# Kernel tuning notes

Measured on AMD Instinct MI355X. Metric: run time of the kernel, lower is better.

## Reference

```python
import jax, jax.numpy as jnp
import numpy as np

NUM_HEADS, NUM_KV, HEAD_DIM, WIDTH = 4, 1, 256, 1024
MASK_FILL = -2.3819763e38


def _apply_rope(x, positions, max_wavelength=10000.0):
    # x: [B, T, N, H], positions: [B, T]
    d = x.shape[-1]
    freq_exp = (2.0 / d) * jnp.arange(d // 2, dtype=jnp.float32)
    timescale = max_wavelength ** freq_exp                      # [H/2]
    radians = positions[..., None].astype(jnp.float32) / timescale  # [B, T, H/2]
    radians = radians[..., None, :]                             # [B, T, 1, H/2]
    sin, cos = jnp.sin(radians), jnp.cos(radians)
    x1, x2 = jnp.split(x, 2, axis=-1)
    out = jnp.concatenate([x1 * cos - x2 * sin, x2 * cos + x1 * sin], axis=-1)
    return out.astype(x.dtype)


def _rmsnorm(x, scale):
    var = jnp.mean(jnp.square(x.astype(jnp.float32)), axis=-1, keepdims=True)
    normed = x * jax.lax.rsqrt(var + 1e-6)
    return (normed * (1 + scale)).astype(x.dtype)


def setup_inputs() -> dict:
    key = jax.random.key(0)
    ks = jax.random.split(key, 7)
    B, T, S = 8, 512, 2048
    return {
        "x": jax.random.normal(ks[0], (B, T, WIDTH), jnp.float32),
        "mem_seq": jax.random.normal(ks[1], (B, S, WIDTH), jnp.float32),
        "mem_mask": jax.random.randint(ks[2], (B, S), 0, 2).astype(bool),
        "rms_scale": jax.random.normal(ks[3], (WIDTH,), jnp.float32) * 0.02,
        "q_w": jax.random.normal(ks[4], (NUM_HEADS, WIDTH, HEAD_DIM), jnp.float32) / np.sqrt(WIDTH),
        "kv_w": jax.random.normal(ks[5], (2, NUM_KV, WIDTH, HEAD_DIM), jnp.float32) / np.sqrt(WIDTH),
        "out_w": jax.random.normal(ks[6], (NUM_HEADS, HEAD_DIM, WIDTH), jnp.float32) / np.sqrt(NUM_HEADS * HEAD_DIM),
    }


def reference(x, mem_seq, mem_mask, rms_scale, q_w, kv_w, out_w):
    B, S, _ = mem_seq.shape
    T = x.shape[1]
    G = NUM_HEADS // NUM_KV  # query heads per kv head

    xn = _rmsnorm(x, rms_scale)          # shared RMSNorm params
    mn = _rmsnorm(mem_seq, rms_scale)

    q = jnp.einsum("BTD,NDH->BTNH", xn, q_w)          # [B,T,4,256]
    kv = jnp.einsum("BSD,cKDH->cBSKH", mn, kv_w)      # [2,B,S,1,256]
    k, v = kv[0], kv[1]

    q_pos = jnp.broadcast_to(jnp.arange(S, T + S), (B, T))
    k_pos = jnp.broadcast_to(jnp.arange(S), (B, S))
    q = _apply_rope(q, q_pos) * (HEAD_DIM ** -0.5)
    k = _apply_rope(k, k_pos)

    q = q.reshape(B, T, NUM_KV, G, HEAD_DIM)
    logits = jnp.einsum("BTKGH,BSKH->BKGTS", q, k, preferred_element_type=jnp.float32)
    masked = jnp.where(mem_mask[:, None, None, None, :], logits, MASK_FILL)
    probs = jax.nn.softmax(masked, axis=-1).astype(x.dtype)
    enc = jnp.einsum("BKGTS,BSKH->BTKGH", probs, v).reshape(B, T, NUM_HEADS, HEAD_DIM)
    return jnp.einsum("BTNH,NHD->BTD", enc, out_w)
```

## Files before the change

### kernel.cpp

```cpp
#include <hip/hip_runtime.h>
#include <stdint.h>

typedef __bf16   bf16x8 __attribute__((ext_vector_type(8)));
typedef float    f32x4  __attribute__((ext_vector_type(4)));
typedef float    f32x16 __attribute__((ext_vector_type(16)));
typedef uint16_t u16x8  __attribute__((ext_vector_type(8)));
typedef uint16_t u16x4  __attribute__((ext_vector_type(4)));
typedef uint32_t u32x4  __attribute__((ext_vector_type(4)));

#define DEVFN static __device__ __forceinline__

DEVFN uint16_t f2bf(float f){
  uint32_t u = __builtin_bit_cast(uint32_t, f);
  u += 0x7fffu + ((u >> 16) & 1u);
  return (uint16_t)(u >> 16);
}
DEVFN float bf2f(uint16_t h){
  return __builtin_bit_cast(float, (uint32_t)h << 16);
}
DEVFN bf16x8 ldbf8(const uint16_t* p){
  return __builtin_bit_cast(bf16x8, *(const u16x8*)p);
}
DEVFN void gl16(const void* g, void* l){
  __builtin_amdgcn_global_load_lds((__attribute__((address_space(1))) void*)g,
                                   (__attribute__((address_space(3))) void*)l,
                                   16, 0, 0);
}
DEVFN f32x4 mfma16(bf16x8 a, bf16x8 b, f32x4 c){
  return __builtin_amdgcn_mfma_f32_16x16x32_bf16(a, b, c, 0, 0, 0);
}
DEVFN f32x16 mfma32(bf16x8 a, bf16x8 b, f32x16 c){
  return __builtin_amdgcn_mfma_f32_32x32x16_bf16(a, b, c, 0, 0, 0);
}
DEVFN uint32_t cvtpk(float lo, float hi){
  uint32_t r;
  asm("v_cvt_pk_bf16_f32 %0, %1, %2" : "=v"(r) : "v"(lo), "v"(hi));
  return r;
}
DEVFN void plswap(uint32_t &x, uint32_t &y){
  asm("v_permlane32_swap_b32 %0, %1" : "+v"(x), "+v"(y));
}
DEVFN int permcol(int j){
  return (((j & 127) >> 4) << 5) + (((j >> 7) & 1) << 4) + (j & 15);
}
DEVFN void fastsc(float rad, float& sn, float& cs){
  float rev = rad * 0.15915494309189535f;
  rev = __builtin_amdgcn_fractf(rev);
  sn = __builtin_amdgcn_sinf(rev);
  cs = __builtin_amdgcn_cosf(rev);
}

__global__ void detect_mask_k(const uint32_t* m, int* flag){
  int i = blockIdx.x * 256 + threadIdx.x;
  uint32_t v = m[i];
  int notint   = (v > 1u) ? 1 : 0;
  int notfloat = (v != 0u && v != 0x3F800000u) ? 2 : 0;
  int bits = notint | notfloat;
  if (__any(bits)){
    int agg = bits;
    agg |= __shfl_xor(agg, 1);  agg |= __shfl_xor(agg, 2);
    agg |= __shfl_xor(agg, 4);  agg |= __shfl_xor(agg, 8);
    agg |= __shfl_xor(agg, 16); agg |= __shfl_xor(agg, 32);
    if ((threadIdx.x & 63) == 0) atomicOr(flag, agg);
  }
}

__global__ __launch_bounds__(256) void fused_pre_k(const float* __restrict__ x,
                                                   const float* __restrict__ mem,
                                                   uint16_t* __restrict__ xn,
                                                   uint16_t* __restrict__ mn,
                                                   const float* __restrict__ scale,
                                                   const float* __restrict__ qw,
                                                   const float* __restrict__ kvw,
                                                   const float* __restrict__ ow,
                                                   uint16_t* __restrict__ wq,
                                                   uint16_t* __restrict__ wkv,
                                                   uint16_t* __restrict__ wout){
  int bid = blockIdx.x;
  if (bid < 20480){
    int row = bid;
    const float* in; uint16_t* out; int r0;
    if (row < 4096){ in = x;  out = xn; r0 = row; }
    else           { in = mem; out = mn; r0 = row - 4096; }
    const float4* ip = (const float4*)(in + (size_t)r0 * 1024);
    float4 v = ip[threadIdx.x];
    float ss = v.x*v.x + v.y*v.y + v.z*v.z + v.w*v.w;
    #pragma unroll
    for (int off = 1; off < 64; off <<= 1) ss += __shfl_xor(ss, off);
    __shared__ float wsum[4];
    if ((threadIdx.x & 63) == 0) wsum[threadIdx.x >> 6] = ss;
    __syncthreads();
    float r = rsqrtf((wsum[0] + wsum[1] + wsum[2] + wsum[3]) * (1.0f/1024.0f) + 1e-6f);
    float4 sc = ((const float4*)scale)[threadIdx.x];
    u16x4 o;
    o[0] = f2bf(v.x * r * (1.0f + sc.x));
    o[1] = f2bf(v.y * r * (1.0f + sc.y));
    o[2] = f2bf(v.z * r * (1.0f + sc.z));
    o[3] = f2bf(v.w * r * (1.0f + sc.w));
    *(u16x4*)(out + (size_t)r0 * 1024 + threadIdx.x * 4) = o;
  } else {
    int t = bid - 20480;
    int z = t >> 10, rem = t & 1023;
    int r0 = (rem >> 5) * 32, c0 = (rem & 31) * 32;
    const float* in; uint16_t* out; int rs, C;
    bool perm;
    if (z < 4)      { in = qw  + z*262144;     out = wq  + z*262144;     rs = 256;  C = 256;  perm = true;  }
    else if (z < 6) { in = kvw + (z-4)*262144; out = wkv + (z-4)*262144; rs = 256;  C = 256;  perm = (z == 4); }
    else            { in = ow;                 out = wout;               rs = 1024; C = 1024; perm = false; }
    if (c0 >= C) return;
    __shared__ float tt[32][33];
    int tx = threadIdx.x & 31, ty = threadIdx.x >> 5;
    #pragma unroll
    for (int i = 0; i < 4; ++i)
      tt[ty + 8*i][tx] = in[(size_t)(r0 + ty + 8*i) * rs + c0 + tx];
    __syncthreads();
    #pragma unroll
    for (int i = 0; i < 4; ++i){
      int c = c0 + ty + 8*i;
      int pc = perm ? permcol(c) : c;
      out[(size_t)pc * 1024 + r0 + tx] = f2bf(tt[tx][ty + 8*i]);
    }
  }
}

#define GEMM_BODY(A_, Bt_, K_)                                                  \
  __shared__ __align__(16) uint16_t As[128*64];                                 \
  __shared__ __align__(16) uint16_t Bs[128*64];                                 \
  f32x4 acc[4][4] = {};                                                         \
  {                                                                             \
    const int K = (K_);                                                         \
    _Pragma("unroll 1")                                                         \
    for (int k0 = 0; k0 < K; k0 += 64){                                         \
      __syncthreads();                                                          \
      _Pragma("unroll")                                                         \
      for (int it = 0; it < 4; ++it){                                           \
        int ob = it * 4096 + tid * 16;                                          \
        int row = ob >> 7;                                                      \
        int col = (ob & 127) ^ ((row & 7) << 4);                                \
        gl16((const char*)(A_)  + ((size_t)(m0 + row) * K + k0) * 2 + col,      \
             (char*)As + it * 4096 + wid * 1024);                               \
        gl16((const char*)(Bt_) + ((size_t)(n0 + row) * K + k0) * 2 + col,      \
             (char*)Bs + it * 4096 + wid * 1024);                               \
      }                                                                         \
      __syncthreads();                                                          \
      bf16x8 af[2][4], bfr[2][4];                                               \
      _Pragma("unroll")                                                         \
      for (int ks = 0; ks < 2; ++ks){                                           \
        _Pragma("unroll")                                                       \
        for (int m = 0; m < 4; ++m)                                             \
          af[ks][m]  = ldbf8(&As[(wr*64 + m*16 + lr) * 64 +                     \
                                 ((ks*32 + lq*8) ^ ((lr & 7) << 3))]);          \
        _Pragma("unroll")                                                       \
        for (int n = 0; n < 4; ++n)                                             \
          bfr[ks][n] = ldbf8(&Bs[(wc*64 + n*16 + lr) * 64 +                     \
                                 ((ks*32 + lq*8) ^ ((lr & 7) << 3))]);          \
      }                                                                         \
      _Pragma("unroll")                                                         \
      for (int ks = 0; ks < 2; ++ks)                                            \
        _Pragma("unroll")                                                       \
        for (int m = 0; m < 4; ++m)                                             \
          _Pragma("unroll")                                                     \
          for (int n = 0; n < 4; ++n)                                           \
            acc[m][n] = mfma16(af[ks][m], bfr[ks][n], acc[m][n]);               \
    }                                                                           \
  }

__global__ __launch_bounds__(256) void gemm_qkv_k(const uint16_t* __restrict__ xn,
                                                  const uint16_t* __restrict__ mn,
                                                  const uint16_t* __restrict__ wq,
                                                  const uint16_t* __restrict__ wkv,
                                                  uint16_t* __restrict__ qb,
                                                  uint16_t* __restrict__ kb,
                                                  uint16_t* __restrict__ vt3){
  int bx = blockIdx.x;
  bool isq = bx < 256;
  const uint16_t *A, *Bt;
  int n0, m0;
  if (isq){
    int m = (bx & 7) + 8 * (bx >> 6);
    int n = (bx >> 3) & 7;
    A = xn; Bt = wq;  n0 = n * 128;  m0 = m * 128;
  } else {
    int b2 = bx - 256;
    int m = (b2 & 7) + 8 * (b2 >> 5);
    int n = (b2 >> 3) & 3;
    A = mn; Bt = wkv; n0 = n * 128; m0 = m * 128;
  }
  int tid = threadIdx.x, lane = tid & 63, wid = tid >> 6;
  int wr = wid >> 1, wc = wid & 1;
  int lr = lane & 15, lq = lane >> 4;
  GEMM_BODY(A, Bt, 1024)
  if (isq){
    #pragma unroll
    for (int m = 0; m < 4; ++m){
      int gr0 = m0 + wr*64 + m*16 + lq*4;
      #pragma unroll
      for (int np = 0; np < 2; ++np){
        int gcl = n0 + wc*64 + (2*np)*16 + lr;
        int j = (((gcl & 255) >> 5) << 4) + (gcl & 15);
        float inv = exp2f((float)j * (-13.287712379549449f / 128.0f));
        #pragma unroll
        for (int r = 0; r < 4; ++r){
          float rad = (float)(2048 + ((gr0 + r) & 511)) * inv;
          float sn, cs; fastsc(rad, sn, cs);
          float x1 = acc[m][2*np][r], x2 = acc[m][2*np + 1][r];
          qb[(size_t)(gr0 + r) * 1024 + gcl]      = f2bf((x1*cs - x2*sn) * 0.0625f);
          qb[(size_t)(gr0 + r) * 1024 + gcl + 16] = f2bf((x2*cs + x1*sn) * 0.0625f);
        }
      }
    }
  } else if (n0 < 256){
    #pragma unroll
    for (int m = 0; m < 4; ++m){
      int gr0 = m0 + wr*64 + m*16 + lq*4;
      #pragma unroll
      for (int np = 0; np < 2; ++np){
        int gcl = n0 + wc*64 + (2*np)*16 + lr;
        int j = ((gcl >> 5) << 4) + (gcl & 15);
        float inv = exp2f((float)j * (-13.287712379549449f / 128.0f));
        #pragma unroll
        for (int r = 0; r < 4; ++r){
          float rad = (float)((gr0 + r) & 2047) * inv;
          float sn, cs; fastsc(rad, sn, cs);
          float x1 = acc[m][2*np][r], x2 = acc[m][2*np + 1][r];
          kb[(size_t)(gr0 + r) * 256 + gcl]      = f2bf(x1*cs - x2*sn);
          kb[(size_t)(gr0 + r) * 256 + gcl + 16] = f2bf(x2*cs + x1*sn);
        }
      }
    }
  } else {
    #pragma unroll
    for (int m = 0; m < 4; ++m)
      #pragma unroll
      for (int n = 0; n < 4; ++n){
        int gr0 = m0 + wr*64 + m*16 + lq*4;
        int gc  = n0 + wc*64 + n*16 + lr;
        int h = gc - 256, bb = gr0 >> 11, s0 = gr0 & 2047;
        int st = s0 >> 5, sc = (s0 >> 3) & 3, s8 = s0 & 7;
        u16x4 pk;
        #pragma unroll
        for (int r = 0; r < 4; ++r) pk[r] = f2bf(acc[m][n][r]);
        *(u16x4*)&vt3[((((size_t)bb*64 + st)*4 + sc)*256 + h)*8 + s8] = pk;
      }
  }
}

__global__ __launch_bounds__(256) void gemm_out_k(const uint16_t* __restrict__ A,
                                                  const uint16_t* __restrict__ Bt,
                                                  float* __restrict__ Cf){
  int bx = blockIdx.x;
  int m = (bx & 7) + 8 * (bx >> 6);
  int n = (bx >> 3) & 7;
  int n0 = n * 128, m0 = m * 128;
  int tid = threadIdx.x, lane = tid & 63, wid = tid >> 6;
  int wr = wid >> 1, wc = wid & 1;
  int lr = lane & 15, lq = lane >> 4;
  GEMM_BODY(A, Bt, 1024)
  #pragma unroll
  for (int mm = 0; mm < 4; ++mm)
    #pragma unroll
    for (int nn = 0; nn < 4; ++nn){
      int gr0 = m0 + wr*64 + mm*16 + lq*4;
      int gc  = n0 + wc*64 + nn*16 + lr;
      #pragma unroll
      for (int r = 0; r < 4; ++r) Cf[(size_t)(gr0 + r) * 1024 + gc] = acc[mm][nn][r];
    }
}

__global__ __launch_bounds__(512, 2) void attn_k(const uint16_t* __restrict__ Q,
                                                 const uint16_t* __restrict__ Kb,
                                                 const uint16_t* __restrict__ Vt3,
                                                 const void* __restrict__ mask,
                                                 const int* __restrict__ flag,
                                                 uint16_t* __restrict__ po,
                                                 uint16_t* __restrict__ po3,
                                                 float* __restrict__ pm,
                                                 float* __restrict__ pl){
  int bx = blockIdx.x;
  int b = bx & 7, qt = (bx >> 3) & 7, sh = bx >> 6;
  int tid = threadIdx.x, lane = tid & 63, wid = tid >> 6;
  int n = wid & 3, qs = wid >> 2;
  int lc = lane & 31, hi = lane >> 5;
  __shared__ __align__(16) uint16_t Ks[3*32*256];
  __shared__ __align__(16) uint16_t Vs[3*4*256*8];
  __shared__ uint32_t mask_lds[16];

  int sbeg = sh * 512;
  {
    int f = *flag;
    int gi = b*2048 + sbeg + tid;
    bool on;
    if ((f & 1) == 0)      on = ((const int*)mask)[gi]    != 0;
    else if ((f & 2) == 0) on = ((const float*)mask)[gi]  != 0.0f;
    else                   on = ((const uint8_t*)mask)[gi] != 0;
    unsigned long long bal = __ballot(on);
    if (lane == 0){
      mask_lds[wid*2]     = (uint32_t)bal;
      mask_lds[wid*2 + 1] = (uint32_t)(bal >> 32);
    }
  }

  int t0w = qt*64 + qs*32;
  bf16x8 qf[16];
  {
    const uint16_t* qp = Q + (size_t)(b*512 + t0w + lc) * 1024 + n*256 + hi*8;
    #pragma unroll
    for (int kc = 0; kc < 16; ++kc) qf[kc] = ldbf8(qp + kc*16);
  }
  f32x16 o[8] = {};
  float mrow = -1e30f, lrow = 0.0f;

  auto STAGE = [&](int buf, int s0){
    const char* vsrc = (const char*)Vt3 + ((size_t)(b*64 + (s0 >> 5))) * 16384;
    #pragma unroll
    for (int it = 0; it < 2; ++it){
      int ob = it*8192 + tid*16;
      int krow = ob >> 9;
      int kcol = (ob & 511) ^ ((krow & 7) << 4);
      gl16((const char*)Kb + ((size_t)(b*2048 + s0 + krow) * 256) * 2 + kcol,
           (char*)Ks + buf*16384 + it*8192 + wid*1024);
      gl16(vsrc + ob,
           (char*)Vs + buf*16384 + it*8192 + wid*1024);
    }
  };

  STAGE(0, sbeg);
  STAGE(1, sbeg + 32);

  #pragma unroll 1
  for (int t = 0; t < 16; ++t){
    if (t == 0)      asm volatile("s_waitcnt vmcnt(4) lgkmcnt(0)" ::: "memory");
    else if (t < 15) asm volatile("s_waitcnt vmcnt(4)" ::: "memory");
    else             asm volatile("s_waitcnt vmcnt(0)" ::: "memory");
    __builtin_amdgcn_s_barrier();
    asm volatile("" ::: "memory");
    if (t < 14) STAGE((t+2)%3, sbeg + (t+2)*32);

    const uint16_t* ksb = Ks + (t%3)*8192;
    const uint16_t* vsb = Vs + (t%3)*8192;

    f32x16 sacc = {};
    __builtin_amdgcn_s_setprio(1);
    #pragma unroll
    for (int kc = 0; kc < 16; ++kc){
      bf16x8 ak = ldbf8(&ksb[lc*256 + ((kc*16 + hi*8) ^ ((lc & 7) << 3))]);
      sacc = mfma32(ak, qf[kc], sacc);
    }
    __builtin_amdgcn_s_setprio(0);

    uint32_t mw = mask_lds[t];
    int sb4 = hi * 4;
    float p[16];
    float mx = -1e30f;
    #pragma unroll
    for (int r = 0; r < 16; ++r){
      int sr = (r & 3) + 8*(r >> 2) + sb4;
      float v = ((mw >> sr) & 1u) ? sacc[r] : -1e30f;
      p[r] = v;
      mx = fmaxf(mx, v);
    }
    mx = fmaxf(mx, __shfl_xor(mx, 32));
    if (__any(mx > mrow + 8.0f)){
      float mn = fmaxf(mrow, mx);
      float scl = __expf(mrow - mn);
      mrow = mn; lrow *= scl;
      #pragma unroll
      for (int ht = 0; ht < 8; ++ht) o[ht] *= scl;
    }
    float rs = 0.0f;
    #pragma unroll
    for (int r = 0; r < 16; ++r){ p[r] = __expf(p[r] - mrow); rs += p[r]; }
    rs += __shfl_xor(rs, 32);
    lrow += rs;

    uint32_t w0, w1, w2, w3, w4, w5, w6, w7;
    w0 = cvtpk(p[0], p[1]);   w2 = cvtpk(p[4], p[5]);   plswap(w0, w2);
    w1 = cvtpk(p[2], p[3]);   w3 = cvtpk(p[6], p[7]);   plswap(w1, w3);
    w4 = cvtpk(p[8], p[9]);   w6 = cvtpk(p[12], p[13]); plswap(w4, w6);
    w5 = cvtpk(p[10], p[11]); w7 = cvtpk(p[14], p[15]); plswap(w5, w7);
    u32x4 t0v = {w0, w1, w2, w3};
    u32x4 t1v = {w4, w5, w6, w7};
    bf16x8 pa0 = __builtin_bit_cast(bf16x8, t0v);
    bf16x8 pa1 = __builtin_bit_cast(bf16x8, t1v);

    __builtin_amdgcn_s_setprio(1);
    #pragma unroll
    for (int ht = 0; ht < 8; ++ht){
      bf16x8 bv0 = ldbf8(&vsb[(size_t)hi*2048       + (ht*32 + lc)*8]);
      o[ht] = mfma32(pa0, bv0, o[ht]);
      bf16x8 bv1 = ldbf8(&vsb[(size_t)(2 + hi)*2048 + (ht*32 + lc)*8]);
      o[ht] = mfma32(pa1, bv1, o[ht]);
    }
    __builtin_amdgcn_s_setprio(0);
  }

  uint16_t* pop = (sh == 3) ? po3 : po + (size_t)sh * 4194304;
  #pragma unroll
  for (int ht = 0; ht < 8; ++ht)
    #pragma unroll
    for (int r = 0; r < 16; ++r){
      int qr = (r & 3) + 8*(r >> 2) + hi*4;
      pop[(size_t)(b*512 + t0w + qr)*1024 + n*256 + ht*32 + lc] = f2bf(o[ht][r]);
    }
  if (hi == 0){
    int mlidx = sh*16384 + (b*512 + t0w + lc)*4 + n;
    pm[mlidx] = mrow;
    pl[mlidx] = lrow;
  }
}

__global__ __launch_bounds__(256) void merge_k(const uint16_t* __restrict__ po,
                                               const uint16_t* __restrict__ po3,
                                               const float* __restrict__ pm,
                                               const float* __restrict__ pl,
                                               uint16_t* __restrict__ enc){
  int idx = blockIdx.x * 4 + (threadIdx.x >> 6);
  int lane = threadIdx.x & 63;
  int row = idx >> 2, n = idx & 3;
  float m = -1e30f;
  #pragma unroll
  for (int h = 0; h < 4; ++h) m = fmaxf(m, pm[h*16384 + idx]);
  float w[4], lsum = 0.0f;
  #pragma unroll
  for (int h = 0; h < 4; ++h){
    w[h] = __expf(pm[h*16384 + idx] - m);
    lsum += pl[h*16384 + idx] * w[h];
  }
  float inv = 1.0f / lsum;
  size_t off = (size_t)row*1024 + n*256 + lane*4;
  float acc[4] = {0.f, 0.f, 0.f, 0.f};
  #pragma unroll
  for (int h = 0; h < 4; ++h){
    const uint16_t* src = (h < 3) ? po + (size_t)h*4194304 + off : po3 + off;
    u16x4 a = *(const u16x4*)src;
    #pragma unroll
    for (int r = 0; r < 4; ++r) acc[r] += bf2f(a[r]) * w[h];
  }
  u16x4 ov;
  #pragma unroll
  for (int r = 0; r < 4; ++r) ov[r] = f2bf(acc[r] * inv);
  *(u16x4*)(enc + off) = ov;
}

extern "C" void kernel_launch(void* const* d_in, const int* in_sizes, int n_in,
                              void* d_out, int out_size, void* d_ws, size_t ws_size,
                              hipStream_t stream){
  const float* x    = (const float*)d_in[0];
  const float* mem  = (const float*)d_in[1];
  const void*  mask = d_in[2];
  const float* rms  = (const float*)d_in[3];
  const float* qw   = (const float*)d_in[4];
  const float* kvw  = (const float*)d_in[5];
  const float* ow   = (const float*)d_in[6];
  float* out = (float*)d_out;
  char* ws = (char*)d_ws;

  uint16_t* xn   = (uint16_t*)(ws + 0);
  uint16_t* enc  = (uint16_t*)(ws + 0);
  const size_t MB = 1ull << 20;
  uint16_t* qb   = (uint16_t*)(ws + 8*MB);
  uint16_t* kb   = (uint16_t*)(ws + 16*MB);
  uint16_t* vt3  = (uint16_t*)(ws + 24*MB);
  uint16_t* wq   = (uint16_t*)(ws + 32*MB);
  float*    pm   = (float*)   (ws + 32*MB);
  float*    pl   = (float*)   (ws + 32*MB + 262144);
  uint16_t* wkv  = (uint16_t*)(ws + 34*MB);
  uint16_t* wout = (uint16_t*)(ws + 35*MB);
  int*      flag = (int*)     (ws + 37*MB);
  uint16_t* mn   = (uint16_t*)(ws + 38*MB);
  uint16_t* po   = (uint16_t*)(ws + 38*MB);
  uint16_t* po3  = (uint16_t*)out;

  hipMemsetAsync(flag, 0, 4, stream);
  detect_mask_k<<<16, 256, 0, stream>>>((const uint32_t*)mask, flag);

  fused_pre_k<<<27648, 256, 0, stream>>>(x, mem, xn, mn, rms, qw, kvw, ow, wq, wkv, wout);

  gemm_qkv_k<<<768, 256, 0, stream>>>(xn, mn, wq, wkv, qb, kb, vt3);

  attn_k<<<256, 512, 0, stream>>>(qb, kb, vt3, mask, flag, po, po3, pm, pl);
  merge_k<<<4096, 256, 0, stream>>>(po, po3, pm, pl, enc);

  gemm_out_k<<<256, 256, 0, stream>>>(enc, wout, out);
}
```

Measured before the change: 161.1 us.

## Fuse split-KV merge into output GEMM and fold mask detection into prep

The separate merge kernel is removed. The output GEMM now computes the per-row combine weights from the partial max and sum values, then merges the four bf16 partial outputs while loading its A tile into LDS. The mask-format detection blocks are appended to the fused preprocessing launch, which drops one kernel launch. All four partials now live in workspace instead of borrowing the output buffer. In exchange, each A tile is merged again by every N-block (8x redundant partial reads), and the A loads become synchronous register loads instead of async global-to-LDS copies.

```diff
diff --git a/kernel.cpp b/kernel.cpp
--- a/kernel.cpp
+++ b/kernel.cpp
@@ -48,21 +48,6 @@
   rev = __builtin_amdgcn_fractf(rev);
   sn = __builtin_amdgcn_sinf(rev);
   cs = __builtin_amdgcn_cosf(rev);
-}
-
-__global__ void detect_mask_k(const uint32_t* m, int* flag){
-  int i = blockIdx.x * 256 + threadIdx.x;
-  uint32_t v = m[i];
-  int notint   = (v > 1u) ? 1 : 0;
-  int notfloat = (v != 0u && v != 0x3F800000u) ? 2 : 0;
-  int bits = notint | notfloat;
-  if (__any(bits)){
-    int agg = bits;
-    agg |= __shfl_xor(agg, 1);  agg |= __shfl_xor(agg, 2);
-    agg |= __shfl_xor(agg, 4);  agg |= __shfl_xor(agg, 8);
-    agg |= __shfl_xor(agg, 16); agg |= __shfl_xor(agg, 32);
-    if ((threadIdx.x & 63) == 0) atomicOr(flag, agg);
-  }
 }
 
 __global__ __launch_bounds__(256) void fused_pre_k(const float* __restrict__ x,
@@ -75,7 +60,9 @@
                                                    const float* __restrict__ ow,
                                                    uint16_t* __restrict__ wq,
                                                    uint16_t* __restrict__ wkv,
-                                                   uint16_t* __restrict__ wout){
+                                                   uint16_t* __restrict__ wout,
+                                                   const uint32_t* __restrict__ mask32,
+                                                   int* __restrict__ flag){
   int bid = blockIdx.x;
   if (bid < 20480){
     int row = bid;
@@ -98,7 +85,7 @@
     o[2] = f2bf(v.z * r * (1.0f + sc.z));
     o[3] = f2bf(v.w * r * (1.0f + sc.w));
     *(u16x4*)(out + (size_t)r0 * 1024 + threadIdx.x * 4) = o;
-  } else {
+  } else if (bid < 27648){
     int t = bid - 20480;
     int z = t >> 10, rem = t & 1023;
     int r0 = (rem >> 5) * 32, c0 = (rem & 31) * 32;
@@ -119,6 +106,19 @@
       int c = c0 + ty + 8*i;
       int pc = perm ? permcol(c) : c;
       out[(size_t)pc * 1024 + r0 + tx] = f2bf(tt[tx][ty + 8*i]);
+    }
+  } else {
+    int i = (bid - 27648) * 256 + threadIdx.x;
+    uint32_t v = mask32[i];
+    int notint   = (v > 1u) ? 1 : 0;
+    int notfloat = (v != 0u && v != 0x3F800000u) ? 2 : 0;
+    int bits = notint | notfloat;
+    if (__any(bits)){
+      int agg = bits;
+      agg |= __shfl_xor(agg, 1);  agg |= __shfl_xor(agg, 2);
+      agg |= __shfl_xor(agg, 4);  agg |= __shfl_xor(agg, 8);
+      agg |= __shfl_xor(agg, 16); agg |= __shfl_xor(agg, 32);
+      if ((threadIdx.x & 63) == 0) atomicOr(flag, agg);
     }
   }
 }
@@ -245,7 +245,9 @@
   }
 }
 
-__global__ __launch_bounds__(256) void gemm_out_k(const uint16_t* __restrict__ A,
+__global__ __launch_bounds__(256) void gemm_out_k(const uint16_t* __restrict__ po,
+                                                  const float* __restrict__ pm,
+                                                  const float* __restrict__ pl,
                                                   const uint16_t* __restrict__ Bt,
                                                   float* __restrict__ Cf){
   int bx = blockIdx.x;
@@ -255,7 +257,76 @@
   int tid = threadIdx.x, lane = tid & 63, wid = tid >> 6;
   int wr = wid >> 1, wc = wid & 1;
   int lr = lane & 15, lq = lane >> 4;
-  GEMM_BODY(A, Bt, 1024)
+  __shared__ __align__(16) uint16_t As[128*64];
+  __shared__ __align__(16) uint16_t Bs[128*64];
+  __shared__ float sc_lds[128][4][4];
+  f32x4 acc[4][4] = {};
+
+  for (int e = tid; e < 512; e += 256){
+    int row = e >> 2, hd = e & 3;
+    int gi = (m0 + row) * 4 + hd;
+    float pmv[4], plv[4], m4 = -1e30f;
+    #pragma unroll
+    for (int h = 0; h < 4; ++h){
+      pmv[h] = pm[h*16384 + gi];
+      plv[h] = pl[h*16384 + gi];
+      m4 = fmaxf(m4, pmv[h]);
+    }
+    float wv[4], ls = 0.0f;
+    #pragma unroll
+    for (int h = 0; h < 4; ++h){ wv[h] = __expf(pmv[h] - m4); ls += plv[h]*wv[h]; }
+    float inv = 1.0f / ls;
+    #pragma unroll
+    for (int h = 0; h < 4; ++h) sc_lds[row][hd][h] = wv[h] * inv;
+  }
+
+  #pragma unroll 1
+  for (int k0 = 0; k0 < 1024; k0 += 64){
+    __syncthreads();
+    int hd = k0 >> 8;
+    #pragma unroll
+    for (int it = 0; it < 4; ++it){
+      int ob = it * 4096 + tid * 16;
+      int row = ob >> 7;
+      int colb = ob & 127;
+      int scolb = colb ^ ((row & 7) << 4);
+      gl16((const char*)Bt + ((size_t)(n0 + row) * 1024 + k0) * 2 + scolb,
+           (char*)Bs + it * 4096 + wid * 1024);
+      size_t abase = ((size_t)(m0 + row) * 1024 + k0) * 2 + colb;
+      u16x8 pp0 = *(const u16x8*)((const char*)po                    + abase);
+      u16x8 pp1 = *(const u16x8*)((const char*)po + (size_t)8388608  + abase);
+      u16x8 pp2 = *(const u16x8*)((const char*)po + (size_t)16777216 + abase);
+      u16x8 pp3 = *(const u16x8*)((const char*)po + (size_t)25165824 + abase);
+      float s0_ = sc_lds[row][hd][0], s1_ = sc_lds[row][hd][1];
+      float s2_ = sc_lds[row][hd][2], s3_ = sc_lds[row][hd][3];
+      u16x8 mrg;
+      #pragma unroll
+      for (int e2 = 0; e2 < 8; ++e2){
+        float a = bf2f(pp0[e2])*s0_ + bf2f(pp1[e2])*s1_
+                + bf2f(pp2[e2])*s2_ + bf2f(pp3[e2])*s3_;
+        mrg[e2] = f2bf(a);
+      }
+      *(u16x8*)((char*)As + row * 128 + scolb) = mrg;
+    }
+    __syncthreads();
+    bf16x8 af[2][4], bfr[2][4];
+    #pragma unroll
+    for (int ks = 0; ks < 2; ++ks){
+      #pragma unroll
+      for (int mm = 0; mm < 4; ++mm)
+        af[ks][mm]  = ldbf8(&As[(wr*64 + mm*16 + lr) * 64 + ((ks*32 + lq*8) ^ ((lr & 7) << 3))]);
+      #pragma unroll
+      for (int nn = 0; nn < 4; ++nn)
+        bfr[ks][nn] = ldbf8(&Bs[(wc*64 + nn*16 + lr) * 64 + ((ks*32 + lq*8) ^ ((lr & 7) << 3))]);
+    }
+    #pragma unroll
+    for (int ks = 0; ks < 2; ++ks)
+      #pragma unroll
+      for (int mm = 0; mm < 4; ++mm)
+        #pragma unroll
+        for (int nn = 0; nn < 4; ++nn)
+          acc[mm][nn] = mfma16(af[ks][mm], bfr[ks][nn], acc[mm][nn]);
+  }
   #pragma unroll
   for (int mm = 0; mm < 4; ++mm)
     #pragma unroll
@@ -273,7 +344,6 @@
                                                  const void* __restrict__ mask,
                                                  const int* __restrict__ flag,
                                                  uint16_t* __restrict__ po,
-                                                 uint16_t* __restrict__ po3,
                                                  float* __restrict__ pm,
                                                  float* __restrict__ pl){
   int bx = blockIdx.x;
@@ -361,9 +431,9 @@
     }
     mx = fmaxf(mx, __shfl_xor(mx, 32));
     if (__any(mx > mrow + 8.0f)){
-      float mn = fmaxf(mrow, mx);
-      float scl = __expf(mrow - mn);
-      mrow = mn; lrow *= scl;
+      float mn2 = fmaxf(mrow, mx);
+      float scl = __expf(mrow - mn2);
+      mrow = mn2; lrow *= scl;
       #pragma unroll
       for (int ht = 0; ht < 8; ++ht) o[ht] *= scl;
     }
@@ -394,7 +464,7 @@
     __builtin_amdgcn_s_setprio(0);
   }
 
-  uint16_t* pop = (sh == 3) ? po3 : po + (size_t)sh * 4194304;
+  uint16_t* pop = po + (size_t)sh * 4194304;
   #pragma unroll
   for (int ht = 0; ht < 8; ++ht)
     #pragma unroll
@@ -407,39 +477,6 @@
     pm[mlidx] = mrow;
     pl[mlidx] = lrow;
   }
-}
-
-__global__ __launch_bounds__(256) void merge_k(const uint16_t* __restrict__ po,
-                                               const uint16_t* __restrict__ po3,
-                                               const float* __restrict__ pm,
-                                               const float* __restrict__ pl,
-                                               uint16_t* __restrict__ enc){
-  int idx = blockIdx.x * 4 + (threadIdx.x >> 6);
-  int lane = threadIdx.x & 63;
-  int row = idx >> 2, n = idx & 3;
-  float m = -1e30f;
-  #pragma unroll
-  for (int h = 0; h < 4; ++h) m = fmaxf(m, pm[h*16384 + idx]);
-  float w[4], lsum = 0.0f;
-  #pragma unroll
-  for (int h = 0; h < 4; ++h){
-    w[h] = __expf(pm[h*16384 + idx] - m);
-    lsum += pl[h*16384 + idx] * w[h];
-  }
-  float inv = 1.0f / lsum;
-  size_t off = (size_t)row*1024 + n*256 + lane*4;
-  float acc[4] = {0.f, 0.f, 0.f, 0.f};
-  #pragma unroll
-  for (int h = 0; h < 4; ++h){
-    const uint16_t* src = (h < 3) ? po + (size_t)h*4194304 + off : po3 + off;
-    u16x4 a = *(const u16x4*)src;
-    #pragma unroll
-    for (int r = 0; r < 4; ++r) acc[r] += bf2f(a[r]) * w[h];
-  }
-  u16x4 ov;
-  #pragma unroll
-  for (int r = 0; r < 4; ++r) ov[r] = f2bf(acc[r] * inv);
-  *(u16x4*)(enc + off) = ov;
 }
 
 extern "C" void kernel_launch(void* const* d_in, const int* in_sizes, int n_in,
@@ -456,7 +493,6 @@
   char* ws = (char*)d_ws;
 
   uint16_t* xn   = (uint16_t*)(ws + 0);
-  uint16_t* enc  = (uint16_t*)(ws + 0);
   const size_t MB = 1ull << 20;
   uint16_t* qb   = (uint16_t*)(ws + 8*MB);
   uint16_t* kb   = (uint16_t*)(ws + 16*MB);
@@ -469,17 +505,15 @@
   int*      flag = (int*)     (ws + 37*MB);
   uint16_t* mn   = (uint16_t*)(ws + 38*MB);
   uint16_t* po   = (uint16_t*)(ws + 38*MB);
-  uint16_t* po3  = (uint16_t*)out;
 
   hipMemsetAsync(flag, 0, 4, stream);
-  detect_mask_k<<<16, 256, 0, stream>>>((const uint32_t*)mask, flag);
-
-  fused_pre_k<<<27648, 256, 0, stream>>>(x, mem, xn, mn, rms, qw, kvw, ow, wq, wkv, wout);
+
+  fused_pre_k<<<27664, 256, 0, stream>>>(x, mem, xn, mn, rms, qw, kvw, ow,
+                                         wq, wkv, wout, (const uint32_t*)mask, flag);
 
   gemm_qkv_k<<<768, 256, 0, stream>>>(xn, mn, wq, wkv, qb, kb, vt3);
 
-  attn_k<<<256, 512, 0, stream>>>(qb, kb, vt3, mask, flag, po, po3, pm, pl);
-  merge_k<<<4096, 256, 0, stream>>>(po, po3, pm, pl, enc);
-
-  gemm_out_k<<<256, 256, 0, stream>>>(enc, wout, out);
-}
+  attn_k<<<256, 512, 0, stream>>>(qb, kb, vt3, mask, flag, po, pm, pl);
+
+  gemm_out_k<<<256, 256, 0, stream>>>(po, pm, pl, wout, out);
+}
```

Result: slower. 175.8 us (+9.1%).
